# Performance work log

Measured on AMD Instinct MI355X. Metric: run time of the kernel, lower is better.

The kernel has to match this reference:

```python
import jax, jax.numpy as jnp
import numpy as np

DIM = 768
NUM_HEADS = 12
DIM_HEAD = 64
INNER = NUM_HEADS * DIM_HEAD  # 768
SCALE = DIM_HEAD ** -0.5


def setup_inputs() -> dict:
    key = jax.random.key(0)
    k1, k2, k3 = jax.random.split(key, 3)
    B, N = 8, 1024
    x = jax.random.normal(k1, (B, N, DIM), dtype=jnp.float32)
    # Linear(dim, 3*inner_dim, bias=False): weight shape (out, in) torch-style
    w_qkv = jax.random.normal(k2, (3 * INNER, DIM), dtype=jnp.float32) * (DIM ** -0.5)
    # proj: Linear(inner_dim, dim, bias=False)
    w_proj = jax.random.normal(k3, (DIM, INNER), dtype=jnp.float32) * (INNER ** -0.5)
    return {"x": x, "w_qkv": w_qkv, "w_proj": w_proj}


def reference(x, w_qkv, w_proj):
    B, N, C = x.shape
    H, dh = NUM_HEADS, DIM_HEAD
    # qkv projection: (B,N,C) @ (C, 3*inner) -> (B,N,3*inner)
    qkv = jnp.einsum('bnc,oc->bno', x, w_qkv)
    qkv = qkv.reshape(B, N, 3, H, dh).transpose(2, 0, 3, 1, 4)  # (3,B,H,N,dh)
    q, k, v = qkv[0], qkv[1], qkv[2]
    # attention scores (B,H,N,N)
    attn_scores = jnp.einsum('bhnd,bhmd->bhnm', q, k) * SCALE
    attn_probs = jax.nn.softmax(attn_scores, axis=-1)
    # attention output (B,H,N,dh) -> (B,N,inner)
    attn_out = jnp.einsum('bhnm,bhmd->bhnd', attn_probs, v)
    attn_out = attn_out.transpose(0, 2, 1, 3).reshape(B, N, H * dh)
    out = jnp.einsum('bni,oi->bno', attn_out, w_proj)
    return out
```

## Files before the change

kernel.cpp:

```cpp
#include <hip/hip_runtime.h>
#include <stdint.h>

typedef unsigned short u16;
typedef __attribute__((ext_vector_type(8))) short short8;
typedef __attribute__((ext_vector_type(4))) short short4v;
typedef __attribute__((ext_vector_type(4))) float f32x4;

#define LOG2E 1.44269504088896340736f

#define Bb 8
#define NSEQ 1024
#define DIMC 768
#define NH 12
#define DH 64
#define INNER 768
#define MTOT (Bb*NSEQ)
#define QKVN (3*INNER)
#define HEADS_TOT (Bb*NH)
#define QKV_PART ((size_t)Bb*NH*NSEQ*DH)

static __device__ inline u16 f2bf(float f) {
    uint32_t u = __builtin_bit_cast(uint32_t, f);
    uint32_t r = (u + 0x7fffu + ((u >> 16) & 1u)) >> 16;
    return (u16)r;
}

static __device__ __forceinline__ uint32_t pkbf(float f0, float f1) {
    uint32_t u0 = __builtin_bit_cast(uint32_t, f0) + 0x8000u;
    uint32_t u1 = __builtin_bit_cast(uint32_t, f1) + 0x8000u;
    return __builtin_amdgcn_perm(u1, u0, 0x07060302u);
}

#if __has_builtin(__builtin_amdgcn_mfma_f32_16x16x16bf16_1k)
static __device__ __forceinline__ f32x4 mfma16(short4v a, short4v b, f32x4 c) {
    return __builtin_amdgcn_mfma_f32_16x16x16bf16_1k(a, b, c, 0, 0, 0);
}
#else
static __device__ __forceinline__ f32x4 mfma16(short4v a, short4v b, f32x4 c) {
    asm volatile("v_mfma_f32_16x16x16_bf16 %0, %1, %2, %0\n\ts_nop 7\n\ts_nop 7"
                 : "+v"(c) : "v"(a), "v"(b));
    return c;
}
#endif

typedef __attribute__((address_space(1))) const void gas_void;
typedef __attribute__((address_space(3))) void las_void;
static __device__ __forceinline__ void async16(u16* lds, const u16* g) {
    __builtin_amdgcn_global_load_lds((gas_void*)(uintptr_t)g,
                                     (las_void*)(uintptr_t)lds, 16, 0, 0);
}

template <int N>
static __device__ __forceinline__ void wait_vm() {
    constexpr int simm = 0x0f70 | (N & 15) | ((N >> 4) << 14);
    __builtin_amdgcn_s_waitcnt(simm);
}

static __device__ __forceinline__ void block_barrier() {
    __builtin_amdgcn_s_barrier();
    __builtin_amdgcn_sched_barrier(0);
}


#define NX8  786432
#define NWQ8 221184
#define NWP8 73728
#define NCVT (NX8 + NWQ8 + NWP8)
__global__ __launch_bounds__(256) void cvt_all(const float* __restrict__ x,
                                               const float* __restrict__ wq,
                                               const float* __restrict__ wp,
                                               u16* __restrict__ xb,
                                               u16* __restrict__ wqb,
                                               u16* __restrict__ wpb) {
    int i = blockIdx.x * 256 + threadIdx.x;
    const float* s; u16* d; int j;
    if (i < NX8) { s = x; d = xb; j = i; }
    else if (i < NX8 + NWQ8) { s = wq; d = wqb; j = i - NX8; }
    else { s = wp; d = wpb; j = i - NX8 - NWQ8; }
    const float4* s4 = (const float4*)s;
    float4 a = s4[2 * j], b = s4[2 * j + 1];
    float v[8] = {a.x, a.y, a.z, a.w, b.x, b.y, b.z, b.w};
    u16 o[8];
#pragma unroll
    for (int t = 0; t < 8; t++) o[t] = f2bf(v[t]);
    ((uint4*)d)[j] = *(const uint4*)o;
}

#define BK 32
__global__ __launch_bounds__(512, 4) void gemm_qkv(const u16* __restrict__ A,
                                                   const u16* __restrict__ Bm,
                                                   u16* __restrict__ qkv) {
    __shared__ u16 As[3][128 * BK];
    __shared__ u16 Bs[3][192 * BK];
    const int tid = threadIdx.x;
    const int w = tid >> 6, lane = tid & 63, quad = lane >> 4, l16 = lane & 15;
    const int wr = w >> 2, wc = w & 3;
    const int bid = blockIdx.x + 12 * blockIdx.y;
    const int xcd = bid & 7, j12 = bid >> 3;
    const int m0 = (8 * xcd + j12 / 12) * 128;
    const int n0 = (j12 % 12) * 192;
    const int K = DIMC;

    const int rl = lane >> 2, cc = lane & 3;
    const int ra = w * 16 + rl;
    const u16* agp = A + (size_t)(m0 + ra) * K + ((cc - ((ra >> 1) & 3)) & 3) * 8;
    const int aslot = (w * 16) * BK;
    const u16* bgp[2]; int bslot[2];
#pragma unroll
    for (int j = 0; j < 2; j++) {
        int rb = j * 128 + w * 16 + rl;
        bgp[j] = Bm + (size_t)(n0 + rb) * K + ((cc - ((rb >> 1) & 3)) & 3) * 8;
        bslot[j] = (j * 128 + w * 16) * BK;
    }
    const bool b2 = (w < 4);

    const int swz = ((quad + ((l16 >> 1) & 3)) & 3) * 8;
    int aoff[4], boff[3];
#pragma unroll
    for (int t = 0; t < 4; t++) aoff[t] = (wr * 64 + t * 16 + l16) * BK + swz;
#pragma unroll
    for (int t = 0; t < 3; t++) boff[t] = (wc * 48 + t * 16 + l16) * BK + swz;

#pragma unroll
    for (int tt = 0; tt < 2; tt++) {
        int kt = tt * BK;
        async16(&As[tt][aslot], agp + kt);
        async16(&Bs[tt][bslot[0]], bgp[0] + kt);
        if (b2) async16(&Bs[tt][bslot[1]], bgp[1] + kt);
    }

    f32x4 acc[4][3] = {};
    const int NIT = K / BK;
    int cur = 0;
    for (int it = 0; it < NIT; ++it) {
        if (it < NIT - 1) {
            if (b2) wait_vm<3>(); else wait_vm<2>();
        } else {
            wait_vm<0>();
        }
        __builtin_amdgcn_s_barrier();
        if (it < NIT - 2) {
            int pre = cur + 2; if (pre >= 3) pre -= 3;
            int ktn = (it + 2) * BK;
            async16(&As[pre][aslot], agp + ktn);
            async16(&Bs[pre][bslot[0]], bgp[0] + ktn);
            if (b2) async16(&Bs[pre][bslot[1]], bgp[1] + ktn);
        }
        short8 af[4], bf[3];
#pragma unroll
        for (int t = 0; t < 4; t++) af[t] = *(const short8*)(&As[cur][aoff[t]]);
#pragma unroll
        for (int t = 0; t < 3; t++) bf[t] = *(const short8*)(&Bs[cur][boff[t]]);
#pragma unroll
        for (int mt = 0; mt < 4; mt++)
#pragma unroll
            for (int nt = 0; nt < 3; nt++)
                acc[mt][nt] = __builtin_amdgcn_mfma_f32_16x16x32_bf16(af[mt], bf[nt],
                                                                      acc[mt][nt], 0, 0, 0);
        cur = (cur == 2) ? 0 : cur + 1;
    }

#pragma unroll
    for (int nt = 0; nt < 3; nt++) {
        int o = n0 + wc * 48 + nt * 16 + l16;
        int which = o / 768;
        int rem = o - which * 768;
        int h = rem >> 6, d = rem & 63;
        if (which == 2) {
            u16* vt = qkv + 2 * QKV_PART;
#pragma unroll
            for (int mt = 0; mt < 4; mt++) {
                int m = m0 + wr * 64 + mt * 16 + quad * 4;
                int bb = m >> 10, ns = m & 1023;
                alignas(8) u16 pk[4];
#pragma unroll
                for (int r = 0; r < 4; r++) pk[r] = f2bf(acc[mt][nt][r]);
                *(uint2*)(vt + ((size_t)(bb * NH + h) * DH + d) * NSEQ + ns) =
                    *(const uint2*)pk;
            }
        } else {
            float sc = (which == 0) ? (0.125f * LOG2E) : 1.0f;
#pragma unroll
            for (int mt = 0; mt < 4; mt++)
#pragma unroll
                for (int r = 0; r < 4; r++) {
                    int m = m0 + wr * 64 + mt * 16 + quad * 4 + r;
                    int bb = m >> 10, ns = m & 1023;
                    size_t idx = (size_t)which * QKV_PART +
                                 (((size_t)(bb * NH + h) * NSEQ + ns) << 6) + d;
                    qkv[idx] = f2bf(acc[mt][nt][r] * sc);
                }
        }
    }
}

#define PBM 64
#define PBN 128
__global__ __launch_bounds__(256, 4) void gemm_proj(const u16* __restrict__ A,
                                                    const u16* __restrict__ Bm,
                                                    float* __restrict__ Co) {
    __shared__ u16 As[PBM * BK];
    __shared__ u16 Bs[PBN * BK];
    const int tid = threadIdx.x;
    const int w = tid >> 6, lane = tid & 63, quad = lane >> 4, l16 = lane & 15;
    const int wr = w >> 1, wc = w & 1;
    const int lin = blockIdx.x + 6 * blockIdx.y;
    const int xcd = lin & 7, j = lin >> 3;
    const int yp = xcd * 16 + j / 6;
    const int xp = j % 6;
    const int m0 = yp * PBM;
    const int n0 = xp * PBN;
    const int K = INNER, N = DIMC;

    const int rl = lane >> 2, cc = lane & 3;
    const int ra = w * 16 + rl;
    const u16* agp = A + (size_t)(m0 + ra) * K + ((cc - ((ra >> 1) & 3)) & 3) * 8;
    const int aslot = (w * 16) * BK;
    const u16* bgp[2]; int bslot[2];
#pragma unroll
    for (int j2 = 0; j2 < 2; j2++) {
        int rb = j2 * 64 + w * 16 + rl;
        bgp[j2] = Bm + (size_t)(n0 + rb) * K + ((cc - ((rb >> 1) & 3)) & 3) * 8;
        bslot[j2] = (j2 * 64 + w * 16) * BK;
    }
    const int swz = ((quad + ((l16 >> 1) & 3)) & 3) * 8;
    int aoff[2], boff[4];
#pragma unroll
    for (int t = 0; t < 2; t++) aoff[t] = (wr * 32 + t * 16 + l16) * BK + swz;
#pragma unroll
    for (int t = 0; t < 4; t++) boff[t] = (wc * 64 + t * 16 + l16) * BK + swz;

    f32x4 acc[2][4] = {};
    const int NIT = K / BK;
    for (int it = 0; it < NIT; ++it) {
        int kt = it * BK;
        async16(&As[aslot], agp + kt);
        async16(&Bs[bslot[0]], bgp[0] + kt);
        async16(&Bs[bslot[1]], bgp[1] + kt);
        __syncthreads();
        short8 af[2], bf[4];
#pragma unroll
        for (int t = 0; t < 2; t++) af[t] = *(const short8*)(&As[aoff[t]]);
#pragma unroll
        for (int t = 0; t < 4; t++) bf[t] = *(const short8*)(&Bs[boff[t]]);
#pragma unroll
        for (int mt = 0; mt < 2; mt++)
#pragma unroll
            for (int nt = 0; nt < 4; nt++)
                acc[mt][nt] = __builtin_amdgcn_mfma_f32_16x16x32_bf16(af[mt], bf[nt],
                                                                      acc[mt][nt], 0, 0, 0);
        __syncthreads();
    }
#pragma unroll
    for (int mt = 0; mt < 2; mt++)
#pragma unroll
        for (int nt = 0; nt < 4; nt++) {
            int o = n0 + wc * 64 + nt * 16 + l16;
#pragma unroll
            for (int r = 0; r < 4; r++) {
                int m = m0 + wr * 32 + mt * 16 + quad * 4 + r;
                Co[(size_t)m * N + o] = acc[mt][nt][r];
            }
        }
}

__global__ __launch_bounds__(256) void attn_kernel(const u16* __restrict__ qkv,
                                                   u16* __restrict__ attn) {
    __shared__ u16 Ks[3][64 * 64];
    __shared__ u16 Vs[3][64 * 64];

    const int tid = threadIdx.x;
    const int w = tid >> 6, lane = tid & 63, quad = lane >> 4, l16 = lane & 15;
    const int bh = blockIdx.x, qt = blockIdx.y;
    const size_t headoff = (size_t)bh * NSEQ * DH;
    const u16* Qp = qkv + headoff;
    const u16* Kp = qkv + QKV_PART + headoff;
    const u16* Vtp = qkv + 2 * QKV_PART + headoff;
    const int q0 = qt * 128 + w * 32;

    const int rl8 = lane >> 3, cc8 = lane & 7;
    const u16* kg[2]; const u16* vg[2]; int ksl[2];
#pragma unroll
    for (int j = 0; j < 2; j++) {
        int r = w * 16 + j * 8 + rl8;
        int c = ((cc8 - r) & 7) * 8;
        kg[j] = Kp + (size_t)r * DH + c;
        vg[j] = Vtp + (size_t)r * NSEQ + c;
        ksl[j] = (w * 16 + j * 8) * 64;
    }

    const int sw0 = ((quad + l16) & 7) * 8;
    const int sw1 = ((quad + 4 + l16) & 7) * 8;

    short8 qf[2][2];
#pragma unroll
    for (int mf = 0; mf < 2; mf++) {
        qf[mf][0] = *(const short8*)(Qp + (size_t)(q0 + mf * 16 + l16) * DH + quad * 8);
        qf[mf][1] = *(const short8*)(Qp + (size_t)(q0 + mf * 16 + l16) * DH + 32 + quad * 8);
    }
    asm volatile("" :: "v"(qf[0][0]), "v"(qf[0][1]), "v"(qf[1][0]), "v"(qf[1][1]));

#pragma unroll
    for (int tt = 0; tt < 3; tt++) {
        int kt = tt * 64;
#pragma unroll
        for (int j = 0; j < 2; j++) {
            async16(&Ks[tt][ksl[j]], kg[j] + (size_t)kt * DH);
            async16(&Vs[tt][ksl[j]], vg[j] + kt);
        }
    }

    f32x4 oacc[2][4] = {};
    float lsum[2] = {0.f, 0.f};

    const int NIT = NSEQ / 64;
    int cur = 0;
    for (int it = 0; it < NIT; ++it) {
        if (it < NIT - 1) wait_vm<4>();
        else              wait_vm<0>();
        block_barrier();
        if (it >= 1 && it < NIT - 2) {
            int pre = cur + 2; if (pre >= 3) pre -= 3;
            int ktn = (it + 2) * 64;
#pragma unroll
            for (int j = 0; j < 2; j++) {
                async16(&Ks[pre][ksl[j]], kg[j] + (size_t)ktn * DH);
                async16(&Vs[pre][ksl[j]], vg[j] + ktn);
            }
        }

        short8 kf[4][2];
#pragma unroll
        for (int nt = 0; nt < 4; nt++) {
            const u16* kr = &Ks[cur][(nt * 16 + l16) * 64];
            kf[nt][0] = *(const short8*)(kr + sw0);
            kf[nt][1] = *(const short8*)(kr + sw1);
        }
        short4v vf[4][4];
#pragma unroll
        for (int nt2 = 0; nt2 < 4; nt2++) {
            int row = nt2 * 16 + l16;
#pragma unroll
            for (int c = 0; c < 4; c++) {
                int off = row * 64 + (((c * 2 + (quad >> 1) + row) & 7) << 3) + (quad & 1) * 4;
                vf[nt2][c] = *(const short4v*)(&Vs[cur][off]);
            }
        }

#pragma unroll
        for (int mf = 0; mf < 2; mf++) {
            f32x4 st[4];
#pragma unroll
            for (int nt = 0; nt < 4; nt++) {
                f32x4 z = {};
                z = __builtin_amdgcn_mfma_f32_16x16x32_bf16(kf[nt][0], qf[mf][0], z, 0, 0, 0);
                z = __builtin_amdgcn_mfma_f32_16x16x32_bf16(kf[nt][1], qf[mf][1], z, 0, 0, 0);
                st[nt] = z;
            }
            short4v pf[4];
#pragma unroll
            for (int c = 0; c < 4; c++) {
                float p0 = __builtin_amdgcn_exp2f(st[c][0]);
                float p1 = __builtin_amdgcn_exp2f(st[c][1]);
                float p2 = __builtin_amdgcn_exp2f(st[c][2]);
                float p3 = __builtin_amdgcn_exp2f(st[c][3]);
                lsum[mf] += (p0 + p1) + (p2 + p3);
                uint2 u = {pkbf(p0, p1), pkbf(p2, p3)};
                pf[c] = __builtin_bit_cast(short4v, u);
            }
#pragma unroll
            for (int nt2 = 0; nt2 < 4; nt2++)
#pragma unroll
                for (int c = 0; c < 4; c++)
                    oacc[mf][nt2] = mfma16(vf[nt2][c], pf[c], oacc[mf][nt2]);
        }
        cur = (cur == 2) ? 0 : cur + 1;
    }

#pragma unroll
    for (int mf = 0; mf < 2; mf++) {
        float v = lsum[mf];
        v += __shfl_xor(v, 16);
        v += __shfl_xor(v, 32);
        lsum[mf] = 1.0f / v;
    }

    const int b = bh / NH, h = bh - (bh / NH) * NH;
#pragma unroll
    for (int mf = 0; mf < 2; mf++) {
        int q = q0 + mf * 16 + l16;
        float inv = lsum[mf];
#pragma unroll
        for (int nt2 = 0; nt2 < 4; nt2++) {
            uint2 u = {pkbf(oacc[mf][nt2][0] * inv, oacc[mf][nt2][1] * inv),
                       pkbf(oacc[mf][nt2][2] * inv, oacc[mf][nt2][3] * inv)};
            int d = nt2 * 16 + quad * 4;
            *(uint2*)(attn + ((size_t)(b * NSEQ + q)) * INNER + h * DH + d) = u;
        }
    }
}

extern "C" void kernel_launch(void* const* d_in, const int* in_sizes, int n_in,
                              void* d_out, int out_size, void* d_ws, size_t ws_size,
                              hipStream_t stream) {
    const float* x = (const float*)d_in[0];
    const float* w_qkv = (const float*)d_in[1];
    const float* w_proj = (const float*)d_in[2];
    float* out = (float*)d_out;

    u16* xb = (u16*)d_ws;
    u16* wqkvb = xb + 6291456;
    u16* wprojb = wqkvb + 1769472;
    u16* qkvb = wprojb + 589824;
    u16* attnb = qkvb + 18874368;

    cvt_all<<<NCVT / 256, 256, 0, stream>>>(x, w_qkv, w_proj, xb, wqkvb, wprojb);

    dim3 g1(QKVN / 192, MTOT / 128);
    gemm_qkv<<<g1, 512, 0, stream>>>(xb, wqkvb, qkvb);

    dim3 g2(HEADS_TOT, NSEQ / 128);
    attn_kernel<<<g2, 256, 0, stream>>>(qkvb, attnb);

    dim3 g3(INNER / PBN, MTOT / PBM);
    gemm_proj<<<g3, 256, 0, stream>>>(attnb, wprojb, out);
}
```

Before: 174.5 us.

## Stage V tiles through registers with XOR swizzle instead of async LDS loads

V tiles are no longer copied straight into LDS with global_load_lds. They are now loaded into registers one tile ahead and written to LDS with a new XOR-based swizzle at 8-byte granularity, and the V fragment reads use the matching swizzle. The goal is fewer LDS bank conflicts on the 4-element V fragment reads. The cost is extra VGPRs and ds_write instructions, plus a wait that also drains lgkm counts. The prologue and prefetch schedule were reworked so K stays async while V goes through registers.

New measurement: 176.1 us. Within noise of the previous version (+0.9%).

```diff
diff --git a/kernel.cpp b/kernel.cpp
--- a/kernel.cpp
+++ b/kernel.cpp
@@ -53,6 +53,11 @@
 template <int N>
 static __device__ __forceinline__ void wait_vm() {
     constexpr int simm = 0x0f70 | (N & 15) | ((N >> 4) << 14);
+    __builtin_amdgcn_s_waitcnt(simm);
+}
+template <int N>
+static __device__ __forceinline__ void wait_vm_lg0() {
+    constexpr int simm = 0x0070 | (N & 15) | ((N >> 4) << 14);
     __builtin_amdgcn_s_waitcnt(simm);
 }
 
@@ -279,14 +284,16 @@
     const int q0 = qt * 128 + w * 32;
 
     const int rl8 = lane >> 3, cc8 = lane & 7;
-    const u16* kg[2]; const u16* vg[2]; int ksl[2];
+    const u16* kg[2]; const u16* vg[2]; int ksl[2], vrow[2], vs0[2];
 #pragma unroll
     for (int j = 0; j < 2; j++) {
         int r = w * 16 + j * 8 + rl8;
-        int c = ((cc8 - r) & 7) * 8;
-        kg[j] = Kp + (size_t)r * DH + c;
-        vg[j] = Vtp + (size_t)r * NSEQ + c;
+        int ck = ((cc8 - r) & 7) * 8;
+        kg[j] = Kp + (size_t)r * DH + ck;
         ksl[j] = (w * 16 + j * 8) * 64;
+        vg[j] = Vtp + (size_t)r * NSEQ + cc8 * 8;
+        vrow[j] = r;
+        vs0[j] = (2 * cc8) ^ (r & 15);
     }
 
     const int sw0 = ((quad + l16) & 7) * 8;
@@ -300,15 +307,37 @@
     }
     asm volatile("" :: "v"(qf[0][0]), "v"(qf[0][1]), "v"(qf[1][0]), "v"(qf[1][1]));
 
-#pragma unroll
-    for (int tt = 0; tt < 3; tt++) {
-        int kt = tt * 64;
+    uint4 vset[2];
+    auto vload = [&](int t) {
+        int kt = t * 64;
+        vset[0] = *(const uint4*)(vg[0] + kt);
+        vset[1] = *(const uint4*)(vg[1] + kt);
+    };
+    auto vwrite = [&](int b) {
 #pragma unroll
         for (int j = 0; j < 2; j++) {
-            async16(&Ks[tt][ksl[j]], kg[j] + (size_t)kt * DH);
-            async16(&Vs[tt][ksl[j]], vg[j] + kt);
-        }
-    }
+            uint2 lo, hi;
+            lo.x = vset[j].x; lo.y = vset[j].y;
+            hi.x = vset[j].z; hi.y = vset[j].w;
+            u16* base = &Vs[b][vrow[j] * 64];
+            *(uint2*)(base + (vs0[j] << 2)) = lo;
+            *(uint2*)(base + ((vs0[j] ^ 1) << 2)) = hi;
+        }
+    };
+
+    vload(0);
+    async16(&Ks[0][ksl[0]], kg[0]);
+    async16(&Ks[0][ksl[1]], kg[1]);
+    wait_vm<2>();
+    vwrite(0);
+    vload(1);
+    async16(&Ks[1][ksl[0]], kg[0] + (size_t)64 * DH);
+    async16(&Ks[1][ksl[1]], kg[1] + (size_t)64 * DH);
+    wait_vm<2>();
+    vwrite(1);
+    vload(2);
+    async16(&Ks[2][ksl[0]], kg[0] + (size_t)128 * DH);
+    async16(&Ks[2][ksl[1]], kg[1] + (size_t)128 * DH);
 
     f32x4 oacc[2][4] = {};
     float lsum[2] = {0.f, 0.f};
@@ -316,16 +345,17 @@
     const int NIT = NSEQ / 64;
     int cur = 0;
     for (int it = 0; it < NIT; ++it) {
-        if (it < NIT - 1) wait_vm<4>();
-        else              wait_vm<0>();
+        if (it < NIT - 1) wait_vm_lg0<2>();
+        else              wait_vm_lg0<0>();
         block_barrier();
-        if (it >= 1 && it < NIT - 2) {
+        if (it + 2 < NIT) {
             int pre = cur + 2; if (pre >= 3) pre -= 3;
-            int ktn = (it + 2) * 64;
-#pragma unroll
-            for (int j = 0; j < 2; j++) {
-                async16(&Ks[pre][ksl[j]], kg[j] + (size_t)ktn * DH);
-                async16(&Vs[pre][ksl[j]], vg[j] + ktn);
+            vwrite(pre);
+            if (it + 3 < NIT) vload(it + 3);
+            if (it >= 1) {
+                int ktn = (it + 2) * 64;
+                async16(&Ks[pre][ksl[0]], kg[0] + (size_t)ktn * DH);
+                async16(&Ks[pre][ksl[1]], kg[1] + (size_t)ktn * DH);
             }
         }
 
@@ -342,7 +372,7 @@
             int row = nt2 * 16 + l16;
 #pragma unroll
             for (int c = 0; c < 4; c++) {
-                int off = row * 64 + (((c * 2 + (quad >> 1) + row) & 7) << 3) + (quad & 1) * 4;
+                int off = row * 64 + ((((c << 2) + quad) ^ l16) << 2);
                 vf[nt2][c] = *(const short4v*)(&Vs[cur][off]);
             }
         }
```
